# Optimization experiments

Measured on AMD Instinct MI355X. Metric: run time of the kernel, lower is better.

## Reference

```python
import jax, jax.numpy as jnp
import numpy as np

V, E, H = 32000, 32, 128
B, T = 2, 512


def setup_inputs() -> dict:
    key = jax.random.key(0)
    ks = jax.random.split(key, 12)
    s = lambda k, shape, scale=0.05: jax.random.normal(k, shape, dtype=jnp.float32) * scale
    return {
        "x": jax.random.randint(ks[0], (B, T), 0, V, dtype=jnp.int64),
        "hidden": jnp.zeros((1, B, H), dtype=jnp.float32),
        "embed_table": s(ks[1], (V, E)),
        "W_ih": s(ks[2], (H, E)),
        "W_hh": s(ks[3], (H, H)),
        "b_ih": jnp.zeros((H,), jnp.float32),
        "b_hh": jnp.zeros((H,), jnp.float32),
        "W1": s(ks[4], (H, H)),
        "W2": s(ks[5], (H, H)),
        "v": s(ks[6], (H,)),
        "Wp": s(ks[7], (H, 2 * H)),
        "bp": jnp.zeros((H,), jnp.float32),
        "Wfc": s(ks[8], (V, H)),
        "bfc": jnp.zeros((V,), jnp.float32),
    }


def reference(x, hidden, embed_table, W_ih, W_hh, b_ih, b_hh, W1, W2, v, Wp, bp, Wfc, bfc):
    # Embedding: (B, T, E)
    emb = embed_table[x]

    # Single-layer tanh RNN (batch_first). Precompute input projections.
    xp = jnp.einsum('bte,he->bth', emb, W_ih) + b_ih + b_hh  # (B,T,H)

    def step(h, x_t):  # h: (B,H), x_t: (B,H)
        h_new = jnp.tanh(x_t + h @ W_hh.T)
        return h_new, h_new

    h0 = hidden[0]  # (B,H)
    h_last, rnn_out = jax.lax.scan(step, h0, jnp.swapaxes(xp, 0, 1))
    rnn_out = jnp.swapaxes(rnn_out, 0, 1)  # (B,T,H)
    hidden_out = h_last[None]  # (1,B,H)

    # Additive (Bahdanau) self-attention with causal mask.
    query = rnn_out @ W1.T  # (B,T,H)
    keys = rnn_out @ W2.T   # (B,T,H)
    # scores: (B,T,T) via (B,T,T,H) broadcast as in the original module
    scores = jnp.einsum('btsh,h->bts', jnp.tanh(query[:, :, None, :] + keys[:, None, :, :]), v)
    causal = jnp.triu(jnp.ones((T, T), bool), k=1)  # mask future s > t
    scores = jnp.where(causal[None], -jnp.inf, scores)
    weights = jax.nn.softmax(scores, axis=-1)
    weights = jnp.nan_to_num(weights)
    context = jnp.einsum('bts,bsh->bth', weights, rnn_out)

    combined = jnp.concatenate([rnn_out, context], axis=-1)  # (B,T,2H)
    out = jax.nn.relu(combined @ Wp.T + bp)  # dropout is identity in eval
    logits = out @ Wfc.T + bfc  # (B,T,V)
    return logits, hidden_out, weights
```

## Files before the change

kernel.cpp:

```cpp
#include <hip/hip_runtime.h>
#include <hip/hip_bf16.h>

#define T 512
#define H 128
#define V 32000
#define B 2
#define CH 64

typedef __attribute__((ext_vector_type(8))) short bf16x8;
typedef __attribute__((ext_vector_type(4))) float f32x4;

__device__ __forceinline__ unsigned short f2bf(float f){
  unsigned int u = __float_as_uint(f);
  u = (u + 0x7FFFu + ((u >> 16) & 1u)) >> 16;
  return (unsigned short)u;
}

__device__ __forceinline__ float fast_tanh(float x){
  float e = __expf(2.f * x);
  return 1.f - __fdividef(2.f, e + 1.f);
}

__device__ __forceinline__ float quad_reduce_add(float x){
  int y1 = __builtin_amdgcn_mov_dpp(__float_as_int(x), 0xB1, 0xF, 0xF, true);
  float s1 = x + __int_as_float(y1);
  int y2 = __builtin_amdgcn_mov_dpp(__float_as_int(s1), 0x4E, 0xF, 0xF, true);
  return s1 + __int_as_float(y2);
}

__device__ __forceinline__ int hswz(int k){
  return ((k >> 2) & 7) * 16 + ((k >> 5) << 2) + (k & 3);
}

__device__ __forceinline__ void gload_lds16(const float* g, float* l){
  __builtin_amdgcn_global_load_lds((const __attribute__((address_space(1))) void*)g,
                                   (__attribute__((address_space(3))) void*)l, 16, 0, 0);
}

__global__ __launch_bounds__(128) void prep_kernel(const int* __restrict__ x,
    const float* __restrict__ table, const float* __restrict__ W_ih,
    const float* __restrict__ b_ih, const float* __restrict__ b_hh,
    float* __restrict__ xp){
  int blk = blockIdx.x;
  int tid = threadIdx.x;
  __shared__ __align__(16) float e[32];
  if (tid < 32) e[tid] = table[(size_t)x[blk] * 32 + tid];
  __syncthreads();
  const float* wr = W_ih + tid * 32;
  float a0 = 0.f, a1 = 0.f, a2 = 0.f, a3 = 0.f;
  #pragma unroll
  for (int k = 0; k < 32; k += 4){
    float4 w4 = *(const float4*)(wr + k);
    float4 e4 = *(const float4*)(e + k);
    a0 += w4.x * e4.x; a1 += w4.y * e4.y; a2 += w4.z * e4.z; a3 += w4.w * e4.w;
  }
  xp[(size_t)blk * H + tid] = (a0 + a1) + (a2 + a3) + b_ih[tid] + b_hh[tid];
}

__global__ __launch_bounds__(256, 1) void rnn_kernel(const float* __restrict__ xp,
    const float* __restrict__ hidden, const float* __restrict__ W_hh,
    const float* __restrict__ Wfc, float* __restrict__ rnn,
    float* __restrict__ hid_out, unsigned short* __restrict__ wfcb){
  if (blockIdx.x >= B){
    size_t base = (size_t)(blockIdx.x - B) * 4096;
    #pragma unroll
    for (int j = 0; j < 4; ++j){
      size_t off = base + (size_t)j * 1024 + (size_t)threadIdx.x * 4;
      float4 f = *(const float4*)(Wfc + off);
      ushort4 o; o.x = f2bf(f.x); o.y = f2bf(f.y); o.z = f2bf(f.z); o.w = f2bf(f.w);
      *(ushort4*)(wfcb + off) = o;
    }
    return;
  }
  int b = blockIdx.x;
  int tid = threadIdx.x;
  int qp = tid >> 2, q = tid & 3;
  int wv = tid >> 6;
  int r0 = 2 * qp;
  const float* wra = W_hh + (size_t)r0 * H + q * 32;
  const float* wrb = wra + H;
  f32x4 A0 = *(const f32x4*)(wra);
  f32x4 A1 = *(const f32x4*)(wra + 4);
  f32x4 A2 = *(const f32x4*)(wra + 8);
  f32x4 A3 = *(const f32x4*)(wra + 12);
  f32x4 A4 = *(const f32x4*)(wra + 16);
  f32x4 A5 = *(const f32x4*)(wra + 20);
  f32x4 A6 = *(const f32x4*)(wra + 24);
  f32x4 A7 = *(const f32x4*)(wra + 28);
  f32x4 B0 = *(const f32x4*)(wrb);
  f32x4 B1 = *(const f32x4*)(wrb + 4);
  f32x4 B2 = *(const f32x4*)(wrb + 8);
  f32x4 B3 = *(const f32x4*)(wrb + 12);
  f32x4 B4 = *(const f32x4*)(wrb + 16);
  f32x4 B5 = *(const f32x4*)(wrb + 20);
  f32x4 B6 = *(const f32x4*)(wrb + 24);
  f32x4 B7 = *(const f32x4*)(wrb + 28);
  asm volatile("" : "+v"(A0), "+v"(A1), "+v"(A2), "+v"(A3),
                    "+v"(A4), "+v"(A5), "+v"(A6), "+v"(A7));
  asm volatile("" : "+v"(B0), "+v"(B1), "+v"(B2), "+v"(B3),
                    "+v"(B4), "+v"(B5), "+v"(B6), "+v"(B7));

  __shared__ __align__(16) float xs[2][CH][H];
  __shared__ __align__(16) float hist[CH][H];
  __shared__ __align__(16) float hb[2][H];

  const float* xpb = xp + (size_t)b * T * H;

  #pragma unroll
  for (int is = 0; is < 8; ++is)
    gload_lds16(xpb + is * 1024 + tid * 4, &xs[0][0][0] + is * 1024 + wv * 256);
  if (tid < H) hb[0][hswz(tid)] = hidden[b * H + tid];
  __syncthreads();

  int wpos = hswz(r0);
  float hn0 = 0.f, hn1 = 0.f;
  int cur = 0, buf = 0;
  for (int chunk = 0; chunk < T / CH; ++chunk){
    if (chunk + 1 < T / CH){
      const float* src = xpb + (size_t)(chunk + 1) * CH * H;
      #pragma unroll
      for (int is = 0; is < 8; ++is)
        gload_lds16(src + is * 1024 + tid * 4, &xs[buf ^ 1][0][0] + is * 1024 + wv * 256);
    }
    for (int s = 0; s < CH; ++s){
      float2 xv = *(const float2*)(&xs[buf][s][r0]);
      const float* hs = &hb[cur][q * 4];
      float a0 = 0.f, a1 = 0.f, b0 = 0.f, b1 = 0.f;
#define FMA8(n) { f32x4 hv = *(const f32x4*)(hs + 16 * n); \
    a0 = fmaf(hv.x, A##n.x, a0); a1 = fmaf(hv.y, A##n.y, a1); \
    a0 = fmaf(hv.z, A##n.z, a0); a1 = fmaf(hv.w, A##n.w, a1); \
    b0 = fmaf(hv.x, B##n.x, b0); b1 = fmaf(hv.y, B##n.y, b1); \
    b0 = fmaf(hv.z, B##n.z, b0); b1 = fmaf(hv.w, B##n.w, b1); }
      FMA8(0) FMA8(1) FMA8(2) FMA8(3) FMA8(4) FMA8(5) FMA8(6) FMA8(7)
#undef FMA8
      float sa = quad_reduce_add(a0 + a1);
      float sb = quad_reduce_add(b0 + b1);
      hn0 = fast_tanh(xv.x + sa);
      hn1 = fast_tanh(xv.y + sb);
      if (q == 0){
        float2 hw; hw.x = hn0; hw.y = hn1;
        *(float2*)(&hb[cur ^ 1][wpos]) = hw;
      }
      if (q == 1){
        float2 hw; hw.x = hn0; hw.y = hn1;
        *(float2*)(&hist[s][r0]) = hw;
      }
      __syncthreads();
      cur ^= 1;
    }
    {
      const float* hsrc = &hist[0][0];
      float* dst = rnn + (size_t)b * T * H + (size_t)chunk * CH * H;
      #pragma unroll
      for (int r = 0; r < 8; ++r)
        *(float4*)(dst + r * 1024 + tid * 4) = *(const float4*)(hsrc + r * 1024 + tid * 4);
    }
    buf ^= 1;
    __syncthreads();
  }
  if (q == 0){
    float2 hw; hw.x = hn0; hw.y = hn1;
    *(float2*)(&hid_out[b * H + r0]) = hw;
  }
}

__global__ __launch_bounds__(256) void qk_kernel(const float* __restrict__ rnn,
    const float* __restrict__ W1, const float* __restrict__ W2,
    float* __restrict__ q, float* __restrict__ ky){
  int bt = blockIdx.x;
  int tid = threadIdx.x;
  __shared__ __align__(16) float r[H];
  if (tid < H) r[tid] = rnn[(size_t)bt * H + tid];
  __syncthreads();
  int i = tid & (H - 1);
  const float* wrow = ((tid < H) ? W1 : W2) + (size_t)i * H;
  float a0 = 0.f, a1 = 0.f, a2 = 0.f, a3 = 0.f;
  #pragma unroll 8
  for (int k = 0; k < H; k += 4){
    float4 w4 = *(const float4*)(wrow + k);
    float4 r4 = *(const float4*)(r + k);
    a0 += w4.x * r4.x; a1 += w4.y * r4.y; a2 += w4.z * r4.z; a3 += w4.w * r4.w;
  }
  float res = (a0 + a1) + (a2 + a3);
  if (tid < H) q[(size_t)bt * H + i] = res;
  else         ky[(size_t)bt * H + i] = res;
}

__global__ __launch_bounds__(256) void attn_kernel(const float* __restrict__ rnn,
    const float* __restrict__ q, const float* __restrict__ ky,
    const float* __restrict__ v, const float* __restrict__ Wp,
    const float* __restrict__ bp, float* __restrict__ wout,
    unsigned short* __restrict__ outb){
  int bt = blockIdx.x;
  int b = bt >> 9, t = bt & (T - 1);
  int tid = threadIdx.x;
  __shared__ __align__(16) float qL[H], vL[H], rrL[H], ctxL[H];
  __shared__ __align__(16) float ctx2[2][H];
  __shared__ __align__(16) float scL[T], wL[T];
  __shared__ float red[4], red2[4];
  if (tid < H){
    qL[tid]  = q[(size_t)bt * H + tid];
    vL[tid]  = v[tid];
    rrL[tid] = rnn[(size_t)bt * H + tid];
  }
  __syncthreads();
  for (int s = tid; s < T; s += 256){
    float sc = -1e30f;
    if (s <= t){
      const float* kr = ky + (size_t)(b * T + s) * H;
      float a0 = 0.f, a1 = 0.f, a2 = 0.f, a3 = 0.f;
      #pragma unroll 4
      for (int h = 0; h < H; h += 4){
        float4 kv = *(const float4*)(kr + h);
        float4 qv = *(const float4*)(qL + h);
        float4 vv = *(const float4*)(vL + h);
        a0 += fast_tanh(qv.x + kv.x) * vv.x;
        a1 += fast_tanh(qv.y + kv.y) * vv.y;
        a2 += fast_tanh(qv.z + kv.z) * vv.z;
        a3 += fast_tanh(qv.w + kv.w) * vv.w;
      }
      sc = (a0 + a1) + (a2 + a3);
    }
    scL[s] = sc;
  }
  __syncthreads();
  float m = -1e30f;
  for (int s = tid; s < T; s += 256) m = fmaxf(m, scL[s]);
  #pragma unroll
  for (int o = 32; o > 0; o >>= 1) m = fmaxf(m, __shfl_xor(m, o));
  if ((tid & 63) == 0) red[tid >> 6] = m;
  __syncthreads();
  float mx = fmaxf(fmaxf(red[0], red[1]), fmaxf(red[2], red[3]));
  float ls = 0.f;
  for (int s = tid; s < T; s += 256){
    float e = (s <= t) ? __expf(scL[s] - mx) : 0.f;
    wL[s] = e; ls += e;
  }
  #pragma unroll
  for (int o = 32; o > 0; o >>= 1) ls += __shfl_xor(ls, o);
  if ((tid & 63) == 0) red2[tid >> 6] = ls;
  __syncthreads();
  float inv = 1.f / (red2[0] + red2[1] + red2[2] + red2[3]);
  for (int s = tid; s < T; s += 256){
    float wv = wL[s] * inv;
    wL[s] = wv;
    wout[(size_t)bt * T + s] = wv;
  }
  __syncthreads();
  {
    int i2 = tid & (H - 1), hf = tid >> 7;
    const float* rb = rnn + (size_t)b * T * H + i2;
    float c0 = 0.f, c1 = 0.f, c2 = 0.f, c3 = 0.f;
    int s = hf;
    for (; s + 6 <= t; s += 8){
      c0 += wL[s]     * rb[(size_t)s * H];
      c1 += wL[s + 2] * rb[(size_t)(s + 2) * H];
      c2 += wL[s + 4] * rb[(size_t)(s + 4) * H];
      c3 += wL[s + 6] * rb[(size_t)(s + 6) * H];
    }
    for (; s <= t; s += 2) c0 += wL[s] * rb[(size_t)s * H];
    ctx2[hf][i2] = (c0 + c1) + (c2 + c3);
  }
  __syncthreads();
  if (tid < H) ctxL[tid] = ctx2[0][tid] + ctx2[1][tid];
  __syncthreads();
  if (tid < H){
    const float* wp = Wp + (size_t)tid * (2 * H);
    float a0 = 0.f, a1 = 0.f, a2 = 0.f, a3 = 0.f;
    #pragma unroll 8
    for (int k = 0; k < H; k += 4){
      float4 w4 = *(const float4*)(wp + k);
      float4 r4 = *(const float4*)(rrL + k);
      a0 += w4.x * r4.x; a1 += w4.y * r4.y; a2 += w4.z * r4.z; a3 += w4.w * r4.w;
    }
    #pragma unroll 8
    for (int k = 0; k < H; k += 4){
      float4 w4 = *(const float4*)(wp + H + k);
      float4 c4 = *(const float4*)(ctxL + k);
      a0 += w4.x * c4.x; a1 += w4.y * c4.y; a2 += w4.z * c4.z; a3 += w4.w * c4.w;
    }
    float o = bp[tid] + (a0 + a1) + (a2 + a3);
    o = fmaxf(o, 0.f);
    outb[(size_t)bt * H + tid] = f2bf(o);
  }
}

__global__ __launch_bounds__(256, 1) void gemm_kernel(const unsigned short* __restrict__ Ab,
    const unsigned short* __restrict__ Bb, const float* __restrict__ bfc,
    float* __restrict__ Cout){
  int tid = threadIdx.x;
  int l = tid & 63, wv = tid >> 6;
  int lm = l & 15, lq = l >> 4;
  int nBase = blockIdx.x * 128;
  __shared__ __align__(16) float cst[64][132];
  bf16x8 bw[32];
  const unsigned short* bp = Bb + (size_t)(nBase + lm) * H + lq * 8;
  #pragma unroll
  for (int sub = 0; sub < 8; ++sub)
    #pragma unroll
    for (int kk = 0; kk < 4; ++kk)
      bw[sub * 4 + kk] = *(const bf16x8*)(bp + (size_t)sub * 16 * H + kk * 32);
  float bias[8];
  #pragma unroll
  for (int sub = 0; sub < 8; ++sub) bias[sub] = bfc[nBase + lm + sub * 16];
  #pragma unroll 1
  for (int mb = 0; mb < 16; ++mb){
    int rowA = mb * 64 + wv * 16 + lm;
    const unsigned short* ap = Ab + (size_t)rowA * H + lq * 8;
    bf16x8 af[4];
    #pragma unroll
    for (int kk = 0; kk < 4; ++kk) af[kk] = *(const bf16x8*)(ap + kk * 32);
    f32x4 acc[8];
    #pragma unroll
    for (int s = 0; s < 8; ++s) acc[s] = (f32x4){0.f, 0.f, 0.f, 0.f};
    #pragma unroll
    for (int kk = 0; kk < 4; ++kk)
      #pragma unroll
      for (int sub = 0; sub < 8; ++sub)
        acc[sub] = __builtin_amdgcn_mfma_f32_16x16x32_bf16(af[kk], bw[sub * 4 + kk], acc[sub], 0, 0, 0);
    int lrow = wv * 16 + lq * 4;
    #pragma unroll
    for (int sub = 0; sub < 8; ++sub)
      #pragma unroll
      for (int r = 0; r < 4; ++r)
        cst[lrow + r][lm + sub * 16] = acc[sub][r] + bias[sub];
    int grow0 = mb * 64 + wv * 16;
    #pragma unroll
    for (int rr = 0; rr < 16; ++rr){
      float2 vv = *(const float2*)(&cst[wv * 16 + rr][l * 2]);
      *(float2*)(&Cout[(size_t)(grow0 + rr) * V + nBase + l * 2]) = vv;
    }
  }
}

extern "C" void kernel_launch(void* const* d_in, const int* in_sizes, int n_in,
                              void* d_out, int out_size, void* d_ws, size_t ws_size,
                              hipStream_t stream){
  const int*   x      = (const int*)d_in[0];
  const float* hidden = (const float*)d_in[1];
  const float* table  = (const float*)d_in[2];
  const float* W_ih   = (const float*)d_in[3];
  const float* W_hh   = (const float*)d_in[4];
  const float* b_ih   = (const float*)d_in[5];
  const float* b_hh   = (const float*)d_in[6];
  const float* W1     = (const float*)d_in[7];
  const float* W2     = (const float*)d_in[8];
  const float* v      = (const float*)d_in[9];
  const float* Wp     = (const float*)d_in[10];
  const float* bp     = (const float*)d_in[11];
  const float* Wfc    = (const float*)d_in[12];
  const float* bfc    = (const float*)d_in[13];

  float* out     = (float*)d_out;
  float* logits  = out;
  float* hid_out = out + (size_t)B * T * V;
  float* w_out   = hid_out + (size_t)B * H;

  float* xp  = (float*)d_ws;
  float* rnn = xp  + (size_t)B * T * H;
  float* q   = rnn + (size_t)B * T * H;
  float* ky  = q   + (size_t)B * T * H;
  unsigned short* outb = (unsigned short*)(ky + (size_t)B * T * H);
  unsigned short* wfcb = outb + (size_t)B * T * H;

  prep_kernel<<<B * T, 128, 0, stream>>>(x, table, W_ih, b_ih, b_hh, xp);
  rnn_kernel<<<B + (V * H) / 4096, 256, 0, stream>>>(xp, hidden, W_hh, Wfc, rnn, hid_out, wfcb);
  qk_kernel<<<B * T, 256, 0, stream>>>(rnn, W1, W2, q, ky);
  attn_kernel<<<B * T, 256, 0, stream>>>(rnn, q, ky, v, Wp, bp, w_out, outb);
  gemm_kernel<<<V / 128, 256, 0, stream>>>(outb, wfcb, bfc, logits);
}
```

Baseline: 444.8 us.

## Split RNN recurrence matvec across 8 lanes per row pair with 512 threads

The sequential RNN kernel now uses 512 threads per block, so each row pair's dot product is split across 8 lanes (16 columns each) instead of 4 lanes (32 columns). The aim is to shorten the serial per-timestep FMA chain and halve the weight registers held per thread. The price is an extra cross-lane shuffle in the reduction and a per-step barrier across 8 waves instead of 4. The hidden-state swizzle, the xp prefetch and the history copy are adjusted to match. The Wfc bf16 conversion blocks are resized to 16384 elements each, giving 250 blocks.

```diff
diff --git a/kernel.cpp b/kernel.cpp
--- a/kernel.cpp
+++ b/kernel.cpp
@@ -28,8 +28,12 @@
   return s1 + __int_as_float(y2);
 }
 
-__device__ __forceinline__ int hswz(int k){
-  return ((k >> 2) & 7) * 16 + ((k >> 5) << 2) + (k & 3);
+__device__ __forceinline__ float cross_quad_add(float x){
+  return x + __shfl_xor(x, 4);
+}
+
+__device__ __forceinline__ int hswz2(int k){
+  return ((k >> 2) & 3) * 32 + ((k >> 4) << 2) + (k & 3);
 }
 
 __device__ __forceinline__ void gload_lds16(const float* g, float* l){
@@ -57,15 +61,15 @@
   xp[(size_t)blk * H + tid] = (a0 + a1) + (a2 + a3) + b_ih[tid] + b_hh[tid];
 }
 
-__global__ __launch_bounds__(256, 1) void rnn_kernel(const float* __restrict__ xp,
+__global__ __launch_bounds__(512, 1) void rnn_kernel(const float* __restrict__ xp,
     const float* __restrict__ hidden, const float* __restrict__ W_hh,
     const float* __restrict__ Wfc, float* __restrict__ rnn,
     float* __restrict__ hid_out, unsigned short* __restrict__ wfcb){
   if (blockIdx.x >= B){
-    size_t base = (size_t)(blockIdx.x - B) * 4096;
-    #pragma unroll
-    for (int j = 0; j < 4; ++j){
-      size_t off = base + (size_t)j * 1024 + (size_t)threadIdx.x * 4;
+    size_t base = (size_t)(blockIdx.x - B) * 16384;
+    #pragma unroll
+    for (int j = 0; j < 8; ++j){
+      size_t off = base + (size_t)j * 2048 + (size_t)threadIdx.x * 4;
       float4 f = *(const float4*)(Wfc + off);
       ushort4 o; o.x = f2bf(f.x); o.y = f2bf(f.y); o.z = f2bf(f.z); o.w = f2bf(f.w);
       *(ushort4*)(wfcb + off) = o;
@@ -74,31 +78,21 @@
   }
   int b = blockIdx.x;
   int tid = threadIdx.x;
-  int qp = tid >> 2, q = tid & 3;
+  int qp = tid >> 3, q = tid & 7;
   int wv = tid >> 6;
   int r0 = 2 * qp;
-  const float* wra = W_hh + (size_t)r0 * H + q * 32;
+  const float* wra = W_hh + (size_t)r0 * H + q * 16;
   const float* wrb = wra + H;
   f32x4 A0 = *(const f32x4*)(wra);
   f32x4 A1 = *(const f32x4*)(wra + 4);
   f32x4 A2 = *(const f32x4*)(wra + 8);
   f32x4 A3 = *(const f32x4*)(wra + 12);
-  f32x4 A4 = *(const f32x4*)(wra + 16);
-  f32x4 A5 = *(const f32x4*)(wra + 20);
-  f32x4 A6 = *(const f32x4*)(wra + 24);
-  f32x4 A7 = *(const f32x4*)(wra + 28);
   f32x4 B0 = *(const f32x4*)(wrb);
   f32x4 B1 = *(const f32x4*)(wrb + 4);
   f32x4 B2 = *(const f32x4*)(wrb + 8);
   f32x4 B3 = *(const f32x4*)(wrb + 12);
-  f32x4 B4 = *(const f32x4*)(wrb + 16);
-  f32x4 B5 = *(const f32x4*)(wrb + 20);
-  f32x4 B6 = *(const f32x4*)(wrb + 24);
-  f32x4 B7 = *(const f32x4*)(wrb + 28);
   asm volatile("" : "+v"(A0), "+v"(A1), "+v"(A2), "+v"(A3),
-                    "+v"(A4), "+v"(A5), "+v"(A6), "+v"(A7));
-  asm volatile("" : "+v"(B0), "+v"(B1), "+v"(B2), "+v"(B3),
-                    "+v"(B4), "+v"(B5), "+v"(B6), "+v"(B7));
+                    "+v"(B0), "+v"(B1), "+v"(B2), "+v"(B3));
 
   __shared__ __align__(16) float xs[2][CH][H];
   __shared__ __align__(16) float hist[CH][H];
@@ -107,34 +101,34 @@
   const float* xpb = xp + (size_t)b * T * H;
 
   #pragma unroll
-  for (int is = 0; is < 8; ++is)
-    gload_lds16(xpb + is * 1024 + tid * 4, &xs[0][0][0] + is * 1024 + wv * 256);
-  if (tid < H) hb[0][hswz(tid)] = hidden[b * H + tid];
-  __syncthreads();
-
-  int wpos = hswz(r0);
+  for (int is = 0; is < 4; ++is)
+    gload_lds16(xpb + is * 2048 + tid * 4, &xs[0][0][0] + wv * 256 + is * 2048);
+  if (tid < H) hb[0][hswz2(tid)] = hidden[b * H + tid];
+  __syncthreads();
+
+  int wpos = hswz2(r0);
   float hn0 = 0.f, hn1 = 0.f;
   int cur = 0, buf = 0;
   for (int chunk = 0; chunk < T / CH; ++chunk){
     if (chunk + 1 < T / CH){
       const float* src = xpb + (size_t)(chunk + 1) * CH * H;
       #pragma unroll
-      for (int is = 0; is < 8; ++is)
-        gload_lds16(src + is * 1024 + tid * 4, &xs[buf ^ 1][0][0] + is * 1024 + wv * 256);
+      for (int is = 0; is < 4; ++is)
+        gload_lds16(src + is * 2048 + tid * 4, &xs[buf ^ 1][0][0] + wv * 256 + is * 2048);
     }
     for (int s = 0; s < CH; ++s){
       float2 xv = *(const float2*)(&xs[buf][s][r0]);
       const float* hs = &hb[cur][q * 4];
       float a0 = 0.f, a1 = 0.f, b0 = 0.f, b1 = 0.f;
-#define FMA8(n) { f32x4 hv = *(const f32x4*)(hs + 16 * n); \
+#define FMA4X(n) { f32x4 hv = *(const f32x4*)(hs + 32 * n); \
     a0 = fmaf(hv.x, A##n.x, a0); a1 = fmaf(hv.y, A##n.y, a1); \
     a0 = fmaf(hv.z, A##n.z, a0); a1 = fmaf(hv.w, A##n.w, a1); \
     b0 = fmaf(hv.x, B##n.x, b0); b1 = fmaf(hv.y, B##n.y, b1); \
     b0 = fmaf(hv.z, B##n.z, b0); b1 = fmaf(hv.w, B##n.w, b1); }
-      FMA8(0) FMA8(1) FMA8(2) FMA8(3) FMA8(4) FMA8(5) FMA8(6) FMA8(7)
-#undef FMA8
-      float sa = quad_reduce_add(a0 + a1);
-      float sb = quad_reduce_add(b0 + b1);
+      FMA4X(0) FMA4X(1) FMA4X(2) FMA4X(3)
+#undef FMA4X
+      float sa = cross_quad_add(quad_reduce_add(a0 + a1));
+      float sb = cross_quad_add(quad_reduce_add(b0 + b1));
       hn0 = fast_tanh(xv.x + sa);
       hn1 = fast_tanh(xv.y + sb);
       if (q == 0){
@@ -149,11 +143,16 @@
       cur ^= 1;
     }
     {
-      const float* hsrc = &hist[0][0];
-      float* dst = rnn + (size_t)b * T * H + (size_t)chunk * CH * H;
-      #pragma unroll
-      for (int r = 0; r < 8; ++r)
-        *(float4*)(dst + r * 1024 + tid * 4) = *(const float4*)(hsrc + r * 1024 + tid * 4);
+      const float* hsrc = &hist[0][0] + tid * 16;
+      float* dst = rnn + (size_t)b * T * H + (size_t)chunk * CH * H + tid * 16;
+      float4 f0 = *(const float4*)(hsrc);
+      float4 f1 = *(const float4*)(hsrc + 4);
+      float4 f2 = *(const float4*)(hsrc + 8);
+      float4 f3 = *(const float4*)(hsrc + 12);
+      *(float4*)(dst)      = f0;
+      *(float4*)(dst + 4)  = f1;
+      *(float4*)(dst + 8)  = f2;
+      *(float4*)(dst + 12) = f3;
     }
     buf ^= 1;
     __syncthreads();
@@ -364,7 +363,7 @@
   unsigned short* wfcb = outb + (size_t)B * T * H;
 
   prep_kernel<<<B * T, 128, 0, stream>>>(x, table, W_ih, b_ih, b_hh, xp);
-  rnn_kernel<<<B + (V * H) / 4096, 256, 0, stream>>>(xp, hidden, W_hh, Wfc, rnn, hid_out, wfcb);
+  rnn_kernel<<<B + 250, 512, 0, stream>>>(xp, hidden, W_hh, Wfc, rnn, hid_out, wfcb);
   qk_kernel<<<B * T, 256, 0, stream>>>(rnn, W1, W2, q, ky);
   attn_kernel<<<B * T, 256, 0, stream>>>(rnn, q, ky, v, Wp, bp, w_out, outb);
   gemm_kernel<<<V / 128, 256, 0, stream>>>(outb, wfcb, bfc, logits);
```

Result: slower. 473.0 us (+6.3%).
